# Kernel tuning notes

Measured on AMD Instinct MI355X. Metric: run time of the kernel, lower is better.

Reference implementation:

```python
import jax, jax.numpy as jnp
import numpy as np

TAG_SIZE = 50
START = TAG_SIZE - 2  # index of '<START>'
STOP = TAG_SIZE - 1   # index of '<STOP>'
B, S = 64, 512


def setup_inputs() -> dict:
    key = jax.random.key(0)
    k1, k2, k3 = jax.random.split(key, 3)
    feats = jax.random.normal(k1, (B, S, TAG_SIZE), dtype=jnp.float32)
    mask = jnp.ones((B, S), dtype=jnp.int32)
    tags = jax.random.randint(k2, (B, S), 0, START)  # valid tags exclude START/STOP
    transitions = jax.random.normal(k3, (TAG_SIZE, TAG_SIZE), dtype=jnp.float32)
    return {"feats": feats, "mask": mask, "tags": tags, "transitions": transitions}


def reference(feats, mask, tags, transitions):
    """CRF neg_log_likelihood_loss = forward_score (log partition, summed) - gold_score.
    feats: (B,S,T) emissions; mask: (B,S) {0,1}; tags: (B,S) gold tags;
    transitions[i,j] = score of transitioning from tag i to tag j.
    """
    b, s, t = feats.shape
    maskf = mask.astype(feats.dtype)

    # ---- forward algorithm (log partition) via scan over time ----
    feats_t = jnp.swapaxes(feats, 0, 1)            # (S,B,T)
    mask_t = jnp.swapaxes(mask, 0, 1).astype(bool)  # (S,B)
    # t=0: partition[b,j] = feats[b,0,j] + transitions[START, j]
    partition0 = feats_t[0] + transitions[START][None, :]  # (B,T)

    def step(partition, xs):
        f_t, m_t = xs  # (B,T), (B,)
        # cur_values[b,i,j] = partition[b,i] + transitions[i,j] + feats[b,t,j]
        cur_values = partition[:, :, None] + transitions[None, :, :] + f_t[:, None, :]
        cur = jax.nn.logsumexp(cur_values, axis=1)  # (B,T) logsumexp over prev tag
        new_partition = jnp.where(m_t[:, None], cur, partition)
        return new_partition, None

    partition, _ = jax.lax.scan(step, partition0, (feats_t[1:], mask_t[1:]))
    terminal = jax.nn.logsumexp(partition[:, :, None] + transitions[None, :, :], axis=1)  # (B,T)
    forward_score = terminal[:, STOP].sum()

    # ---- gold score ----
    # prev tag at step 0 is START, otherwise tags[:, t-1]
    prev = jnp.concatenate([jnp.full((b, 1), START, dtype=tags.dtype), tags[:, :-1]], axis=1)
    emit = jnp.take_along_axis(feats, tags[..., None], axis=2)[..., 0]  # (B,S)
    trans = transitions[prev, tags]                                      # (B,S)
    tg_energy = ((emit + trans) * maskf).sum()
    lengths = mask.astype(jnp.int32).sum(axis=1)                         # (B,)
    end_ids = jnp.take_along_axis(tags, (lengths - 1)[:, None].astype(tags.dtype), axis=1)[:, 0]
    end_energy = transitions[end_ids, STOP].sum()
    gold_score = tg_energy + end_energy

    return forward_score - gold_score
```

## Files before the change

kernel.cpp:

```cpp
#include <hip/hip_runtime.h>
#include <hip/hip_bf16.h>

#define T 50
#define NB 64
#define NS 512
#define START_TAG 48
#define STOP_TAG 49

typedef _Float16 f16_t;
typedef _Float16 f16x2 __attribute__((ext_vector_type(2)));
typedef _Float16 f16x4 __attribute__((ext_vector_type(4)));
typedef float    f32x4 __attribute__((ext_vector_type(4)));

static constexpr float LOG2E = 1.4426950408889634f;
static constexpr float LN2F  = 0.6931471805599453f;
static constexpr float S_E   = 6.0f;
#define NEG_BIG (-1.0e38f)

__device__ __forceinline__ float fexp2(float x) { return __builtin_amdgcn_exp2f(x); }
__device__ __forceinline__ float flog2(float x) { return __builtin_amdgcn_logf(x); }
__device__ __forceinline__ f16x2 bcast_h2(f16x2 v, int src) {
    unsigned u = __builtin_amdgcn_readlane(__builtin_bit_cast(unsigned, v), src);
    return __builtin_bit_cast(f16x2, u);
}
__device__ __forceinline__ f16x2 pack_h2(float a, float b) {
    return __builtin_bit_cast(f16x2, __builtin_amdgcn_cvt_pkrtz(a, b));
}

__device__ __forceinline__ float wave_fmax_dpp(float x) {
#define DPP_STEP(ctrl)                                                        \
    do {                                                                      \
        int _s = __builtin_bit_cast(int, x);                                  \
        int _p = __builtin_amdgcn_update_dpp(_s, _s, (ctrl), 0xf, 0xf, false);\
        x = fmaxf(x, __builtin_bit_cast(float, _p));                          \
    } while (0)
    DPP_STEP(0x111);
    DPP_STEP(0x112);
    DPP_STEP(0x114);
    DPP_STEP(0x118);
    DPP_STEP(0x142);
    DPP_STEP(0x143);
#undef DPP_STEP
    return __builtin_bit_cast(float,
        __builtin_amdgcn_readlane(__builtin_bit_cast(int, x), 63));
}

template<int NCHT, int CHLT>
__global__ __launch_bounds__(256, 6)
void crf_chunk(const float* __restrict__ feats, const int* __restrict__ mask,
               const float* __restrict__ trans, f16_t* __restrict__ wsCt,
               float* __restrict__ wsD) {
    const int c    = blockIdx.x;
    const int b    = blockIdx.y;
    const int tid  = threadIdx.x;
    const int w    = tid >> 6;
    const int lane = tid & 63;
    const int l15  = lane & 15;
    const int q    = lane >> 4;

    __shared__ float sF[CHLT][64];
    __shared__ f16_t Ml[64 * 72];

    const int t0  = c * CHLT + 1;
    const int nst = (NS - t0 < CHLT) ? (NS - t0) : CHLT;

    f16x4 Afrag[4][4];
    #pragma unroll
    for (int mb = 0; mb < 4; mb++)
        #pragma unroll
        for (int kb = 0; kb < 4; kb++) {
            f16x4 v;
            #pragma unroll
            for (int j = 0; j < 4; j++) {
                const int kk = 16 * kb + 4 * q + j;
                const int mm = 16 * mb + l15;
                float x = 0.f;
                if (kk < T && mm < T) x = fexp2(fmaf(trans[kk * T + mm], LOG2E, -S_E));
                v[j] = (f16_t)x;
            }
            Afrag[mb][kb] = v;
        }

    for (int r = w; r < CHLT; r += 4) {
        int tl = t0 + r; tl = tl < NS ? tl : NS - 1;
        float fv = (lane < T && r < nst) ? feats[((size_t)b * NS + tl) * T + lane] : 0.f;
        sF[r][lane] = (lane < T && r < nst) ? fexp2(fv * LOG2E) : 0.f;
    }

    unsigned long long bm;
    {
        int tl = t0 + lane; tl = tl < NS ? tl : NS - 1;
        int mv = (lane < nst) ? mask[b * NS + tl] : 0;
        bm = __ballot(mv != 0);
    }
    __syncthreads();

    f16x4 Bt[4];
    #pragma unroll
    for (int rb = 0; rb < 4; rb++) {
        f16x4 v;
        #pragma unroll
        for (int j = 0; j < 4; j++)
            v[j] = (f16_t)((rb == w && 4 * q + j == l15) ? 1.f : 0.f);
        Bt[rb] = v;
    }

    float D  = 0.f;
    float m1 = 1.f, m2 = 1.f;

    for (int s = 0; s < nst; s++) {
        if ((bm >> s) & 1ull) {
            int ebits = (int)((__float_as_uint(m2) >> 23) & 255) - 127;
            ebits = ebits > 14 ? 14 : (ebits < -14 ? -14 : ebits);
            const float descale = __uint_as_float((unsigned)(127 - ebits) << 23);
            D += (float)ebits + S_E;

            const f32x4 zz = {0.f, 0.f, 0.f, 0.f};
            f32x4 acc[4];
            #pragma unroll
            for (int mb = 0; mb < 4; mb++)
                acc[mb] = __builtin_amdgcn_mfma_f32_16x16x16f16(Afrag[mb][0], Bt[0], zz, 0, 0, 0);
            #pragma unroll
            for (int kb = 1; kb < 4; kb++)
                #pragma unroll
                for (int mb = 0; mb < 4; mb++)
                    acc[mb] = __builtin_amdgcn_mfma_f32_16x16x16f16(Afrag[mb][kb], Bt[kb], acc[mb], 0, 0, 0);

            float wm = 0.f;
            #pragma unroll
            for (int mb = 0; mb < 4; mb++) {
                f32x4 cs = *(const f32x4*)&sF[s][16 * mb + 4 * q];
                f32x4 csd;
                #pragma unroll
                for (int r = 0; r < 4; r++) csd[r] = cs[r] * descale;
                float v0 = acc[mb][0] * csd[0];
                float v1 = acc[mb][1] * csd[1];
                float v2 = acc[mb][2] * csd[2];
                float v3 = acc[mb][3] * csd[3];
                wm = fmaxf(wm, fmaxf(fmaxf(v0, v1), fmaxf(v2, v3)));
                f16x4 hv;
                hv[0] = (f16_t)v0; hv[1] = (f16_t)v1;
                hv[2] = (f16_t)v2; hv[3] = (f16_t)v3;
                Bt[mb] = hv;
            }

            m2 = m1;
            m1 = wave_fmax_dpp(wm);
        }
    }

    {
        const int P2 = 72;
        #pragma unroll
        for (int rb = 0; rb < 4; rb++) {
            f16x4 v = Bt[rb];
            #pragma unroll
            for (int r = 0; r < 4; r++)
                Ml[(16 * rb + 4 * q + r) * P2 + 16 * w + l15] = v[r];
        }
        __syncthreads();
        const int row = tid >> 2;
        const int seg = tid & 3;
        const f16_t* src = &Ml[row * P2 + seg * 16];
        f16_t* dst = wsCt + ((size_t)(b * NCHT + c)) * 4096 + row * 64 + seg * 16;
        ((int4*)dst)[0] = *(const int4*)&src[0];
        ((int4*)dst)[1] = *(const int4*)&src[8];
    }
    if (lane == 0) wsD[(b * NCHT + c) * 4 + w] = D;
}

template<int NCHT>
__global__ __launch_bounds__(128, 1)
void crf_combine(const float* __restrict__ feats, const int* __restrict__ mask,
                 const int* __restrict__ tags, const float* __restrict__ trans,
                 const f16_t* __restrict__ wsCt, const float* __restrict__ wsD,
                 float* __restrict__ out) {
    const int b    = blockIdx.x;
    const int tid  = threadIdx.x;
    const int wv   = tid >> 6;
    const int lane = tid & 63;

    __shared__ float sGold;
    float fwd = 0.f;

    if (wv == 1) {
        float gsum = 0.f;
        int   lcnt = 0;
        for (int s = lane; s < NS; s += 64) {
            int   m  = mask[b * NS + s];
            int   tg = tags[b * NS + s];
            int   pv = (s == 0) ? START_TAG : tags[b * NS + s - 1];
            float e  = feats[((size_t)b * NS + s) * T + tg];
            float tr = trans[pv * T + tg];
            if (m) { gsum += e + tr; lcnt += 1; }
        }
        #pragma unroll
        for (int off = 32; off > 0; off >>= 1) {
            gsum += __shfl_down(gsum, off, 64);
            lcnt += __shfl_down(lcnt, off, 64);
        }
        if (lane == 0) sGold = gsum + trans[tags[b * NS + lcnt - 1] * T + STOP_TAG];
    } else {
        float part = (lane < T)
            ? (feats[(size_t)b * NS * T + lane] + trans[START_TAG * T + lane]) * LOG2E
            : NEG_BIG;

        float Dq[NCHT];
        #pragma unroll
        for (int cc = 0; cc < NCHT; cc++)
            Dq[cc] = wsD[(b * NCHT + cc) * 4 + (lane >> 4)];

        int bufA[32], bufB[32];
        {
            const f16_t* src = wsCt + (size_t)b * NCHT * 4096 + lane * 64;
            #pragma unroll
            for (int kk = 0; kk < 8; kk++)
                *(int4*)&bufA[4 * kk] = ((const int4*)src)[kk];
        }

        auto cbody = [&](int (&cur)[32], int (&nxt)[32], int cc) {
            if (cc + 1 < NCHT) {
                const f16_t* src = wsCt + (size_t)(b * NCHT + cc + 1) * 4096 + lane * 64;
                #pragma unroll
                for (int kk = 0; kk < 8; kk++)
                    *(int4*)&nxt[4 * kk] = ((const int4*)src)[kk];
            }

            float tmp = part + Dq[cc];
            float sft = wave_fmax_dpp(tmp);
            float ex  = fexp2(tmp - sft);
            float exo = __shfl_xor(ex, 1, 64);
            f16x2 pk  = pack_h2(ex, exo);

            float a0 = 0.f, a1 = 0.f, a2 = 0.f, a3 = 0.f;
            #pragma unroll
            for (int k = 0; k < 25; k += 4) {
                a0 = __builtin_amdgcn_fdot2(bcast_h2(pk, 2 * k), __builtin_bit_cast(f16x2, cur[k]), a0, false);
                if (k + 1 < 25) a1 = __builtin_amdgcn_fdot2(bcast_h2(pk, 2 * (k + 1)), __builtin_bit_cast(f16x2, cur[k + 1]), a1, false);
                if (k + 2 < 25) a2 = __builtin_amdgcn_fdot2(bcast_h2(pk, 2 * (k + 2)), __builtin_bit_cast(f16x2, cur[k + 2]), a2, false);
                if (k + 3 < 25) a3 = __builtin_amdgcn_fdot2(bcast_h2(pk, 2 * (k + 3)), __builtin_bit_cast(f16x2, cur[k + 3]), a3, false);
            }
            part = sft + flog2((a0 + a1) + (a2 + a3));
        };

        #pragma unroll
        for (int p = 0; p < NCHT / 2; p++) {
            cbody(bufA, bufB, 2 * p);
            cbody(bufB, bufA, 2 * p + 1);
        }

        float v = (lane < T) ? part + trans[lane * T + STOP_TAG] * LOG2E : NEG_BIG;
        float mx = wave_fmax_dpp(v);
        float ee = (lane < T) ? fexp2(v - mx) : 0.f;
        #pragma unroll
        for (int off = 32; off > 0; off >>= 1) ee += __shfl_xor(ee, off, 64);
        fwd = (mx + flog2(ee)) * LN2F;
    }

    __syncthreads();
    if (tid == 0) atomicAdd(out, fwd - sGold);
}

extern "C" void kernel_launch(void* const* d_in, const int* in_sizes, int n_in,
                              void* d_out, int out_size, void* d_ws, size_t ws_size,
                              hipStream_t stream) {
    const float* feats = (const float*)d_in[0];
    const int*   mask  = (const int*)d_in[1];
    const int*   tags  = (const int*)d_in[2];
    const float* trans = (const float*)d_in[3];
    float* out = (float*)d_out;

    (void)hipMemsetAsync(out, 0, sizeof(float) * out_size, stream);

    const size_t matBytes16 = (size_t)NB * 16 * 4096 * sizeof(f16_t);
    const size_t need16     = matBytes16 + (size_t)NB * 16 * 4 * sizeof(float);

    if (ws_size >= need16) {
        f16_t* wsCt = (f16_t*)d_ws;
        float* wsD  = (float*)((char*)d_ws + matBytes16);
        crf_chunk<16, 32><<<dim3(16, NB), 256, 0, stream>>>(feats, mask, trans, wsCt, wsD);
        crf_combine<16><<<NB, 128, 0, stream>>>(feats, mask, tags, trans, wsCt, wsD, out);
    } else {
        const size_t matBytes8 = (size_t)NB * 8 * 4096 * sizeof(f16_t);
        f16_t* wsCt = (f16_t*)d_ws;
        float* wsD  = (float*)((char*)d_ws + matBytes8);
        crf_chunk<8, 64><<<dim3(8, NB), 256, 0, stream>>>(feats, mask, trans, wsCt, wsD);
        crf_combine<8><<<NB, 128, 0, stream>>>(feats, mask, tags, trans, wsCt, wsD, out);
    }
}
```

Measured before the change: 107.3 us.

## Interleave two independent chunk chains per block to hide MFMA latency

Adds a crf_chunk2 kernel in which each block runs two 16-step chunk recurrences side by side, interleaving their MFMA chains so one chain's latency can be covered by the other's work. The launch picks 32 chunks of 16 steps when the workspace allows it, which shortens the serial chunk phase but doubles the number of matrices the combine kernel has to chain through. Launch bounds drop from 6 to 4 waves per SIMD to make room for the extra register state.

```diff
diff --git a/kernel.cpp b/kernel.cpp
--- a/kernel.cpp
+++ b/kernel.cpp
@@ -45,8 +45,195 @@
         __builtin_amdgcn_readlane(__builtin_bit_cast(int, x), 63));
 }
 
+template<int NPAIR, int CHLT>
+__global__ __launch_bounds__(256, 4)
+void crf_chunk2(const float* __restrict__ feats, const int* __restrict__ mask,
+                const float* __restrict__ trans, f16_t* __restrict__ wsCt,
+                float* __restrict__ wsD) {
+    const int p    = blockIdx.x;
+    const int b    = blockIdx.y;
+    const int tid  = threadIdx.x;
+    const int w    = tid >> 6;
+    const int lane = tid & 63;
+    const int l15  = lane & 15;
+    const int q    = lane >> 4;
+    const int NCHT = 2 * NPAIR;
+
+    __shared__ float sF[2 * CHLT][64];
+    __shared__ f16_t Ml[64 * 72];
+
+    const int cA  = 2 * p;
+    const int t0A = cA * CHLT + 1;
+
+    f16x4 Afrag[4][4];
+    #pragma unroll
+    for (int mb = 0; mb < 4; mb++)
+        #pragma unroll
+        for (int kb = 0; kb < 4; kb++) {
+            f16x4 v;
+            #pragma unroll
+            for (int j = 0; j < 4; j++) {
+                const int kk = 16 * kb + 4 * q + j;
+                const int mm = 16 * mb + l15;
+                float x = 0.f;
+                if (kk < T && mm < T) x = fexp2(fmaf(trans[kk * T + mm], LOG2E, -S_E));
+                v[j] = (f16_t)x;
+            }
+            Afrag[mb][kb] = v;
+        }
+
+    for (int r = w; r < 2 * CHLT; r += 4) {
+        int tl = t0A + r;
+        bool val = (tl < NS) && (lane < T);
+        tl = tl < NS ? tl : NS - 1;
+        float fv = val ? feats[((size_t)b * NS + tl) * T + lane] : 0.f;
+        sF[r][lane] = val ? fexp2(fv * LOG2E) : 0.f;
+    }
+
+    unsigned bmA, bmB;
+    {
+        int g = t0A + lane;
+        int mv = (lane < 2 * CHLT && g < NS) ? mask[b * NS + g] : 0;
+        unsigned long long bm = __ballot(mv != 0);
+        bmA = (unsigned)(bm & ((1ull << CHLT) - 1));
+        bmB = (unsigned)((bm >> CHLT) & ((1ull << CHLT) - 1));
+    }
+    __syncthreads();
+
+    f16x4 BtA[4], BtB[4];
+    #pragma unroll
+    for (int rb = 0; rb < 4; rb++) {
+        f16x4 v;
+        #pragma unroll
+        for (int j = 0; j < 4; j++)
+            v[j] = (f16_t)((rb == w && 4 * q + j == l15) ? 1.f : 0.f);
+        BtA[rb] = v; BtB[rb] = v;
+    }
+
+    float DA = 0.f, DB = 0.f;
+    float m1A = 1.f, m2A = 1.f, m1B = 1.f, m2B = 1.f;
+
+    const f32x4 zz = {0.f, 0.f, 0.f, 0.f};
+
+    for (int s = 0; s < CHLT; s++) {
+        const bool doA = (bmA >> s) & 1u;
+        const bool doB = (bmB >> s) & 1u;
+
+        float dscA = 1.f, dscB = 1.f;
+        if (doA) {
+            int e = (int)((__float_as_uint(m2A) >> 23) & 255) - 127;
+            e = e > 14 ? 14 : (e < -14 ? -14 : e);
+            dscA = __uint_as_float((unsigned)(127 - e) << 23);
+            DA += (float)e + S_E;
+        }
+        if (doB) {
+            int e = (int)((__float_as_uint(m2B) >> 23) & 255) - 127;
+            e = e > 14 ? 14 : (e < -14 ? -14 : e);
+            dscB = __uint_as_float((unsigned)(127 - e) << 23);
+            DB += (float)e + S_E;
+        }
+
+        f32x4 accA[4], accB[4];
+        if (doA) {
+            #pragma unroll
+            for (int mb = 0; mb < 4; mb++)
+                accA[mb] = __builtin_amdgcn_mfma_f32_16x16x16f16(Afrag[mb][0], BtA[0], zz, 0, 0, 0);
+        }
+        if (doB) {
+            #pragma unroll
+            for (int mb = 0; mb < 4; mb++)
+                accB[mb] = __builtin_amdgcn_mfma_f32_16x16x16f16(Afrag[mb][0], BtB[0], zz, 0, 0, 0);
+        }
+        #pragma unroll
+        for (int kb = 1; kb < 4; kb++) {
+            if (doA) {
+                #pragma unroll
+                for (int mb = 0; mb < 4; mb++)
+                    accA[mb] = __builtin_amdgcn_mfma_f32_16x16x16f16(Afrag[mb][kb], BtA[kb], accA[mb], 0, 0, 0);
+            }
+            if (doB) {
+                #pragma unroll
+                for (int mb = 0; mb < 4; mb++)
+                    accB[mb] = __builtin_amdgcn_mfma_f32_16x16x16f16(Afrag[mb][kb], BtB[kb], accB[mb], 0, 0, 0);
+            }
+        }
+
+        if (doA) {
+            float wm = 0.f;
+            #pragma unroll
+            for (int mb = 0; mb < 4; mb++) {
+                f32x4 cs = *(const f32x4*)&sF[s][16 * mb + 4 * q];
+                float v0 = accA[mb][0] * (cs[0] * dscA);
+                float v1 = accA[mb][1] * (cs[1] * dscA);
+                float v2 = accA[mb][2] * (cs[2] * dscA);
+                float v3 = accA[mb][3] * (cs[3] * dscA);
+                wm = fmaxf(wm, fmaxf(fmaxf(v0, v1), fmaxf(v2, v3)));
+                f16x4 hv;
+                hv[0] = (f16_t)v0; hv[1] = (f16_t)v1;
+                hv[2] = (f16_t)v2; hv[3] = (f16_t)v3;
+                BtA[mb] = hv;
+            }
+            m2A = m1A; m1A = wave_fmax_dpp(wm);
+        }
+        if (doB) {
+            float wm = 0.f;
+            #pragma unroll
+            for (int mb = 0; mb < 4; mb++) {
+                f32x4 cs = *(const f32x4*)&sF[CHLT + s][16 * mb + 4 * q];
+                float v0 = accB[mb][0] * (cs[0] * dscB);
+                float v1 = accB[mb][1] * (cs[1] * dscB);
+                float v2 = accB[mb][2] * (cs[2] * dscB);
+                float v3 = accB[mb][3] * (cs[3] * dscB);
+                wm = fmaxf(wm, fmaxf(fmaxf(v0, v1), fmaxf(v2, v3)));
+                f16x4 hv;
+                hv[0] = (f16_t)v0; hv[1] = (f16_t)v1;
+                hv[2] = (f16_t)v2; hv[3] = (f16_t)v3;
+                BtB[mb] = hv;
+            }
+            m2B = m1B; m1B = wave_fmax_dpp(wm);
+        }
+    }
+
+    const int P2  = 72;
+    const int row = tid >> 2;
+    const int seg = tid & 3;
+    {
+        #pragma unroll
+        for (int rb = 0; rb < 4; rb++) {
+            f16x4 v = BtA[rb];
+            #pragma unroll
+            for (int r = 0; r < 4; r++)
+                Ml[(16 * rb + 4 * q + r) * P2 + 16 * w + l15] = v[r];
+        }
+        __syncthreads();
+        const f16_t* src = &Ml[row * P2 + seg * 16];
+        f16_t* dst = wsCt + ((size_t)(b * NCHT + cA)) * 4096 + row * 64 + seg * 16;
+        ((int4*)dst)[0] = *(const int4*)&src[0];
+        ((int4*)dst)[1] = *(const int4*)&src[8];
+        __syncthreads();
+    }
+    {
+        #pragma unroll
+        for (int rb = 0; rb < 4; rb++) {
+            f16x4 v = BtB[rb];
+            #pragma unroll
+            for (int r = 0; r < 4; r++)
+                Ml[(16 * rb + 4 * q + r) * P2 + 16 * w + l15] = v[r];
+        }
+        __syncthreads();
+        const f16_t* src = &Ml[row * P2 + seg * 16];
+        f16_t* dst = wsCt + ((size_t)(b * NCHT + cA + 1)) * 4096 + row * 64 + seg * 16;
+        ((int4*)dst)[0] = *(const int4*)&src[0];
+        ((int4*)dst)[1] = *(const int4*)&src[8];
+    }
+    if (lane == 0) {
+        wsD[(b * NCHT + cA) * 4 + w]     = DA;
+        wsD[(b * NCHT + cA + 1) * 4 + w] = DB;
+    }
+}
+
 template<int NCHT, int CHLT>
-__global__ __launch_bounds__(256, 6)
+__global__ __launch_bounds__(256, 4)
 void crf_chunk(const float* __restrict__ feats, const int* __restrict__ mask,
                const float* __restrict__ trans, f16_t* __restrict__ wsCt,
                float* __restrict__ wsD) {
@@ -130,13 +317,10 @@
             #pragma unroll
             for (int mb = 0; mb < 4; mb++) {
                 f32x4 cs = *(const f32x4*)&sF[s][16 * mb + 4 * q];
-                f32x4 csd;
-                #pragma unroll
-                for (int r = 0; r < 4; r++) csd[r] = cs[r] * descale;
-                float v0 = acc[mb][0] * csd[0];
-                float v1 = acc[mb][1] * csd[1];
-                float v2 = acc[mb][2] * csd[2];
-                float v3 = acc[mb][3] * csd[3];
+                float v0 = acc[mb][0] * (cs[0] * descale);
+                float v1 = acc[mb][1] * (cs[1] * descale);
+                float v2 = acc[mb][2] * (cs[2] * descale);
+                float v3 = acc[mb][3] * (cs[3] * descale);
                 wm = fmaxf(wm, fmaxf(fmaxf(v0, v1), fmaxf(v2, v3)));
                 f16x4 hv;
                 hv[0] = (f16_t)v0; hv[1] = (f16_t)v1;
@@ -244,9 +428,9 @@
         };
 
         #pragma unroll
-        for (int p = 0; p < NCHT / 2; p++) {
-            cbody(bufA, bufB, 2 * p);
-            cbody(bufB, bufA, 2 * p + 1);
+        for (int pp = 0; pp < NCHT / 2; pp++) {
+            cbody(bufA, bufB, 2 * pp);
+            cbody(bufB, bufA, 2 * pp + 1);
         }
 
         float v = (lane < T) ? part + trans[lane * T + STOP_TAG] * LOG2E : NEG_BIG;
@@ -272,10 +456,17 @@
 
     (void)hipMemsetAsync(out, 0, sizeof(float) * out_size, stream);
 
+    const size_t matBytes32 = (size_t)NB * 32 * 4096 * sizeof(f16_t);
+    const size_t need32     = matBytes32 + (size_t)NB * 32 * 4 * sizeof(float);
     const size_t matBytes16 = (size_t)NB * 16 * 4096 * sizeof(f16_t);
     const size_t need16     = matBytes16 + (size_t)NB * 16 * 4 * sizeof(float);
 
-    if (ws_size >= need16) {
+    if (ws_size >= need32) {
+        f16_t* wsCt = (f16_t*)d_ws;
+        float* wsD  = (float*)((char*)d_ws + matBytes32);
+        crf_chunk2<16, 16><<<dim3(16, NB), 256, 0, stream>>>(feats, mask, trans, wsCt, wsD);
+        crf_combine<32><<<NB, 128, 0, stream>>>(feats, mask, tags, trans, wsCt, wsD, out);
+    } else if (ws_size >= need16) {
         f16_t* wsCt = (f16_t*)d_ws;
         float* wsD  = (float*)((char*)d_ws + matBytes16);
         crf_chunk<16, 32><<<dim3(16, NB), 256, 0, stream>>>(feats, mask, trans, wsCt, wsD);
```

New measurement: 117.2 us. +9.2%, slower.
